# Kernel optimization log

Measured on AMD Instinct MI355X. Metric: run time of the kernel, lower is better.

Reference implementation:

```python
import jax, jax.numpy as jnp
import numpy as np

EPS = 1e-6
NUM_HEADS = 16

def _rmsnorm(h, w):
    hf = h.astype(jnp.float32)
    var = jnp.mean(hf * hf, axis=-1, keepdims=True)
    return (w * (hf * jax.lax.rsqrt(var + EPS))).astype(h.dtype)

def _rotary(t, cos, sin):
    # t: [B,N,H,hd]; cos/sin: [N, hd//2]
    tf = t.astype(jnp.float32)
    tr = tf[..., 0::2]
    ti = tf[..., 1::2]
    c = cos[None, :, None, :]
    s = sin[None, :, None, :]
    out_r = tr * c - ti * s
    out_i = tr * s + ti * c
    out = jnp.stack([out_r, out_i], axis=-1).reshape(t.shape)
    return out.astype(t.dtype)

def setup_inputs() -> dict:
    key = jax.random.key(0)
    ks = jax.random.split(key, 8)
    B, N, C = 2, 2048, 1024
    hd = C // NUM_HEADS
    x = jax.random.normal(ks[0], (B, N, C), jnp.float32)
    qkv_w = jax.random.normal(ks[1], (3 * C, C), jnp.float32) * (C ** -0.5)
    q_norm_w = jnp.ones((hd,), jnp.float32)
    k_norm_w = jnp.ones((hd,), jnp.float32)
    proj_w = jax.random.normal(ks[2], (C, C), jnp.float32) * (C ** -0.5)
    proj_b = jnp.zeros((C,), jnp.float32)
    # rotary freqs_cis = exp(i * theta): unit-magnitude cos/sin
    inv_freq = 1.0 / (10000.0 ** (jnp.arange(0, hd, 2, dtype=jnp.float32) / hd))
    ang = jnp.arange(N, dtype=jnp.float32)[:, None] * inv_freq[None, :]
    pos_cos = jnp.cos(ang)
    pos_sin = jnp.sin(ang)
    mask = jnp.tril(jnp.ones((N, N), dtype=bool))
    return {"x": x, "qkv_w": qkv_w, "q_norm_w": q_norm_w, "k_norm_w": k_norm_w,
            "proj_w": proj_w, "proj_b": proj_b, "pos_cos": pos_cos,
            "pos_sin": pos_sin, "mask": mask}

def reference(x, qkv_w, q_norm_w, k_norm_w, proj_w, proj_b, pos_cos, pos_sin, mask):
    B, N, C = x.shape
    H = NUM_HEADS
    hd = C // H
    qkv = (x @ qkv_w.T).reshape(B, N, 3, H, hd)
    q, k, v = qkv[:, :, 0], qkv[:, :, 1], qkv[:, :, 2]  # [B,N,H,hd]
    q = _rmsnorm(q, q_norm_w)
    k = _rmsnorm(k, k_norm_w)
    q = _rotary(q, pos_cos, pos_sin)
    k = _rotary(k, pos_cos, pos_sin)
    q = q.transpose(0, 2, 1, 3)  # [B,H,N,hd]
    k = k.transpose(0, 2, 1, 3)
    v = v.transpose(0, 2, 1, 3)
    scale = hd ** -0.5
    scores = jnp.einsum('bhqd,bhkd->bhqk', q, k) * scale
    scores = jnp.where(mask[None, None, :, :], scores, jnp.float32(-1e30))
    attn = jax.nn.softmax(scores, axis=-1)
    out = jnp.einsum('bhqk,bhkd->bhqd', attn, v)
    out = out.transpose(0, 2, 1, 3).reshape(B, N, C)
    return out @ proj_w.T + proj_b
```

## Files before the change

kernel.cpp:

```cpp
#include <hip/hip_runtime.h>

using u16 = unsigned short;
using short4v = __attribute__((ext_vector_type(4))) short;
using short8 = __attribute__((ext_vector_type(8))) short;
using floatx4 = __attribute__((ext_vector_type(4))) float;

__device__ __forceinline__ float bf2f(u16 h) {
  union { unsigned int u; float f; } v;
  v.u = ((unsigned int)h) << 16;
  return v.f;
}
__device__ __forceinline__ u16 f2bf(float f) {
  union { float f; unsigned int u; } v;
  v.f = f;
  unsigned int u = v.u;
  return (u16)((u + 0x7FFFu + ((u >> 16) & 1u)) >> 16);
}
__device__ __forceinline__ u16 f2bf_rtz(float f) {
  union { float f; unsigned int u; } v;
  v.f = f;
  return (u16)(v.u >> 16);
}

__device__ __forceinline__ float exp2_raw(float x) {
  return __builtin_amdgcn_exp2f(x);
}
__device__ __forceinline__ float rcp_raw(float x) {
  return __builtin_amdgcn_rcpf(x);
}

typedef const __attribute__((address_space(1))) unsigned int* gas_t;
typedef __attribute__((address_space(3))) unsigned int* las_t;
__device__ __forceinline__ void gl_lds16(const u16* g, u16* l) {
  __builtin_amdgcn_global_load_lds((gas_t)(const void*)g, (las_t)(void*)l, 16,
                                   0, 0);
}

#define MFMA32 __builtin_amdgcn_mfma_f32_16x16x32_bf16

#define QSCALE 0.180336880111f

__global__ __launch_bounds__(256) void cvt_all(
    const float* __restrict__ x, const float* __restrict__ wq,
    const float* __restrict__ wp, u16* __restrict__ xb, u16* __restrict__ wqb,
    u16* __restrict__ wpb) {
  int i = blockIdx.x * 256 + threadIdx.x;
  const float* src;
  u16* dst;
  int off;
  if (i < 1048576) {
    src = x; dst = xb; off = i;
  } else if (i < 1048576 + 786432) {
    src = wq; dst = wqb; off = i - 1048576;
  } else {
    src = wp; dst = wpb; off = i - 1835008;
  }
  float4 v = ((const float4*)src)[off];
  ushort4 o;
  o.x = f2bf(v.x);
  o.y = f2bf(v.y);
  o.z = f2bf(v.z);
  o.w = f2bf(v.w);
  ((ushort4*)dst)[off] = o;
}

template <int BIAS, int OUTBF16, int MT>
__global__ __launch_bounds__(256) void gemm_nt(
    const u16* __restrict__ A, const u16* __restrict__ B,
    const float* __restrict__ bias, void* __restrict__ Cout,
    int M, int N, int K) {
  constexpr int ROWS_A = MT * 32;
  __shared__ u16 As[ROWS_A * 64];
  __shared__ u16 Bs[128 * 64];
  const int tid = threadIdx.x;
  const int lane = tid & 63;
  const int wave = tid >> 6;
  const int col = lane & 15;
  const int quad = lane >> 4;
  const int bm = blockIdx.y * ROWS_A;
  const int bn = blockIdx.x * 128;
  const int wm = (wave >> 1) * (MT * 16);
  const int wn = (wave & 1) * 64;
  const int rsw = col & 7;

  floatx4 acc[MT][4] = {};

  for (int kb = 0; kb < K; kb += 64) {
    __syncthreads();
#pragma unroll
    for (int c = tid; c < ROWS_A * 8; c += 256) {
      const int row = c >> 3, s = (c & 7) ^ (row & 7);
      gl_lds16(A + (size_t)(bm + row) * K + kb + s * 8, As + c * 8);
    }
#pragma unroll
    for (int c = tid; c < 1024; c += 256) {
      const int row = c >> 3, s = (c & 7) ^ (row & 7);
      gl_lds16(B + (size_t)(bn + row) * K + kb + s * 8, Bs + c * 8);
    }
    __syncthreads();

#pragma unroll
    for (int kk = 0; kk < 2; kk++) {
      short8 af[MT], bfr[4];
#pragma unroll
      for (int i = 0; i < MT; i++)
        af[i] = *(const short8*)(As + (wm + i * 16 + col) * 64 +
                                 ((kk * 4 + quad) ^ rsw) * 8);
#pragma unroll
      for (int i = 0; i < 4; i++)
        bfr[i] = *(const short8*)(Bs + (wn + i * 16 + col) * 64 +
                                  ((kk * 4 + quad) ^ rsw) * 8);
#pragma unroll
      for (int mi = 0; mi < MT; mi++)
#pragma unroll
        for (int ni = 0; ni < 4; ni++)
          acc[mi][ni] = MFMA32(af[mi], bfr[ni], acc[mi][ni], 0, 0, 0);
    }
  }

#pragma unroll
  for (int mi = 0; mi < MT; mi++) {
#pragma unroll
    for (int ni = 0; ni < 4; ni++) {
#pragma unroll
      for (int r = 0; r < 4; r++) {
        int row = bm + wm + mi * 16 + quad * 4 + r;
        int c = bn + wn + ni * 16 + col;
        float v = acc[mi][ni][r];
        if (BIAS) v += bias[c];
        if (OUTBF16)
          ((u16*)Cout)[(size_t)row * N + c] = f2bf(v);
        else
          ((float*)Cout)[(size_t)row * N + c] = v;
      }
    }
  }
}

__global__ __launch_bounds__(256) void rope_v(
    const u16* __restrict__ qkv, const float* __restrict__ qw,
    const float* __restrict__ kw, const float* __restrict__ pcos,
    const float* __restrict__ psin, u16* __restrict__ Qb,
    u16* __restrict__ Kb, u16* __restrict__ Vt) {
  __shared__ u16 T[64 * 68];
  const int bh = blockIdx.x;
  const int n0 = blockIdx.y * 64;
  const int b = bh >> 4, h = bh & 15;
  const int tid = threadIdx.x;
  const int lane = tid & 63;
  const int wave = tid >> 6;

  const float qwl = qw[lane];
  const float kwl = kw[lane];
  for (int tt = 0; tt < 16; tt++) {
    const int n = n0 + wave * 16 + tt;
    const int t = b * 2048 + n;
    const u16* base = qkv + (size_t)t * 3072 + h * 64 + lane;
    float qv = bf2f(base[0]);
    float kv = bf2f(base[1024]);

    float sq = qv * qv, sk = kv * kv;
#pragma unroll
    for (int off = 32; off; off >>= 1) {
      sq += __shfl_xor(sq, off);
      sk += __shfl_xor(sk, off);
    }
    float qn = qv * rsqrtf(sq * (1.0f / 64.0f) + 1e-6f) * qwl;
    float kn = kv * rsqrtf(sk * (1.0f / 64.0f) + 1e-6f) * kwl;

    const int i = lane >> 1;
    const float c = pcos[n * 32 + i];
    const float s = psin[n * 32 + i];
    float qp = __shfl_xor(qn, 1);
    float kp = __shfl_xor(kn, 1);
    float qr, kr;
    if (lane & 1) {
      qr = qp * s + qn * c;
      kr = kp * s + kn * c;
    } else {
      qr = qn * c - qp * s;
      kr = kn * c - kp * s;
    }
    qr *= QSCALE;

    const size_t o = ((size_t)bh * 2048 + n) * 64 + lane;
    Qb[o] = f2bf(qr);
    Kb[o] = f2bf(kr);
  }

  const int q = tid & 7;
  const int r = tid >> 3;
#pragma unroll
  for (int rr = r; rr < 64; rr += 32) {
    short8 v = *(const short8*)(qkv + (size_t)(b * 2048 + n0 + rr) * 3072 +
                                2048 + h * 64 + q * 8);
    *(short8*)&T[rr * 68 + q * 8] = v;
  }
  __syncthreads();
#pragma unroll
  for (int dd = r; dd < 64; dd += 32) {
    short8 o;
#pragma unroll
    for (int j = 0; j < 8; j++) o[j] = T[(q * 8 + j) * 68 + dd];
    *(short8*)(Vt + (size_t)(bh * 64 + dd) * 2048 + n0 + q * 8) = o;
  }
}

__global__ __launch_bounds__(256) void attn_flash(
    const u16* __restrict__ Q, const u16* __restrict__ Kk,
    const u16* __restrict__ Vt, u16* __restrict__ O) {
  __shared__ u16 Ks[2][2][64 * 32];
  __shared__ u16 Vs[2][2][64 * 32];
  __shared__ u16 Pb[4][16 * 64];
  const int id = blockIdx.x;
  const int bh = id & 31;
  const int tile = 31 - (id >> 5);
  const int tid = threadIdx.x;
  const int lane = tid & 63;
  const int wave = tid >> 6;
  const int col = lane & 15;
  const int quad = lane >> 4;
  const int srow = tid >> 2;
  const int sswz = ((tid & 3) ^ (srow & 3)) * 8;
  const int rq = (quad ^ (col & 3)) * 8;
  const int pswz = (col & 7) << 1;

  const u16* Qh = Q + (size_t)bh * 2048 * 64;
  const u16* Kh = Kk + (size_t)bh * 2048 * 64;
  const u16* Vh = Vt + (size_t)bh * 64 * 2048;
  const int b = bh >> 4, h = bh & 15;

  const int q0 = tile * 64 + wave * 16;

  short8 aq[2];
#pragma unroll
  for (int ks = 0; ks < 2; ks++)
    aq[ks] = *(const short8*)(Qh + (size_t)(q0 + col) * 64 + ks * 32 + quad * 8);

  short8 ones;
#pragma unroll
  for (int j = 0; j < 8; j++) ones[j] = (short)0x3F80;

  floatx4 accO[4] = {};
  floatx4 lacc = {};
  const int nsteps = tile + 1;

#pragma unroll
  for (int half = 0; half < 2; half++) {
    gl_lds16(Kh + (size_t)srow * 64 + half * 32 + sswz,
             &Ks[0][half][0] + tid * 8);
    gl_lds16(Vh + (size_t)srow * 2048 + half * 32 + sswz,
             &Vs[0][half][0] + tid * 8);
  }
  __syncthreads();

  int cur = 0;
  for (int kt = 0; kt < nsteps; kt++) {
    const int j0 = kt * 64;

    if (kt + 1 < nsteps) {
      const int j1 = j0 + 64;
#pragma unroll
      for (int half = 0; half < 2; half++) {
        gl_lds16(Kh + (size_t)(j1 + srow) * 64 + half * 32 + sswz,
                 &Ks[cur ^ 1][half][0] + tid * 8);
        gl_lds16(Vh + (size_t)srow * 2048 + j1 + half * 32 + sswz,
                 &Vs[cur ^ 1][half][0] + tid * 8);
      }
    }

    floatx4 s[4] = {};
#pragma unroll
    for (int nt = 0; nt < 4; nt++) {
#pragma unroll
      for (int ks = 0; ks < 2; ks++) {
        short8 bk = *(const short8*)&Ks[cur][ks][(nt * 16 + col) * 32 + rq];
        s[nt] = MFMA32(bk, aq[ks], s[nt], 0, 0, 0);
      }
    }

    if (j0 + 63 <= q0) {
#pragma unroll
      for (int nt = 0; nt < 4; nt++) {
        short4v pk;
#pragma unroll
        for (int r = 0; r < 4; r++)
          pk[r] = (short)f2bf_rtz(exp2_raw(s[nt][r]));
        *(short4v*)&Pb[wave][col * 64 + ((nt * 4 + quad) ^ pswz) * 4] = pk;
      }
    } else {
      const int qg = q0 + col;
#pragma unroll
      for (int nt = 0; nt < 4; nt++) {
        const int jgb = j0 + nt * 16 + quad * 4;
        short4v pk;
#pragma unroll
        for (int r = 0; r < 4; r++) {
          float pv = (jgb + r <= qg) ? exp2_raw(s[nt][r]) : 0.0f;
          pk[r] = (short)f2bf_rtz(pv);
        }
        *(short4v*)&Pb[wave][col * 64 + ((nt * 4 + quad) ^ pswz) * 4] = pk;
      }
    }

    short8 ap[2];
#pragma unroll
    for (int kf = 0; kf < 2; kf++)
      ap[kf] = *(const short8*)&Pb[wave][col * 64 +
                                         ((kf * 8 + quad * 2) ^ pswz) * 4];

#pragma unroll
    for (int kf = 0; kf < 2; kf++)
      lacc = MFMA32(ap[kf], ones, lacc, 0, 0, 0);

#pragma unroll
    for (int nt = 0; nt < 4; nt++) {
#pragma unroll
      for (int kf = 0; kf < 2; kf++) {
        short8 bv = *(const short8*)&Vs[cur][kf][(nt * 16 + col) * 32 + rq];
        accO[nt] = MFMA32(ap[kf], bv, accO[nt], 0, 0, 0);
      }
    }

    __syncthreads();
    cur ^= 1;
  }

  float lrec[4];
#pragma unroll
  for (int r = 0; r < 4; r++) lrec[r] = rcp_raw(lacc[r]);

#pragma unroll
  for (int nt = 0; nt < 4; nt++) {
#pragma unroll
    for (int r = 0; r < 4; r++) {
      int qg = q0 + quad * 4 + r;
      int d = nt * 16 + col;
      O[((size_t)(b * 2048 + qg) * 16 + h) * 64 + d] =
          f2bf(accO[nt][r] * lrec[r]);
    }
  }
}

extern "C" void kernel_launch(void* const* d_in, const int* in_sizes, int n_in,
                              void* d_out, int out_size, void* d_ws,
                              size_t ws_size, hipStream_t stream) {
  const float* x = (const float*)d_in[0];
  const float* qkv_w = (const float*)d_in[1];
  const float* q_norm_w = (const float*)d_in[2];
  const float* k_norm_w = (const float*)d_in[3];
  const float* proj_w = (const float*)d_in[4];
  const float* proj_b = (const float*)d_in[5];
  const float* pos_cos = (const float*)d_in[6];
  const float* pos_sin = (const float*)d_in[7];

  char* ws = (char*)d_ws;
  u16* xb = (u16*)ws;
  u16* wqkvb = (u16*)(ws + 8388608);
  u16* wprojb = (u16*)(ws + 14680064);
  u16* qkv = (u16*)(ws + 16777216);
  u16* Qb = (u16*)(ws + 41943040);
  u16* Kb = (u16*)(ws + 50331648);
  u16* Vt = (u16*)(ws + 58720256);
  u16* AO = (u16*)(ws + 67108864);

  cvt_all<<<8192, 256, 0, stream>>>(x, qkv_w, proj_w, xb, wqkvb, wprojb);

  gemm_nt<0, 1, 4><<<dim3(24, 32), 256, 0, stream>>>(xb, wqkvb, nullptr, qkv,
                                                     4096, 3072, 1024);

  rope_v<<<dim3(32, 32), 256, 0, stream>>>(qkv, q_norm_w, k_norm_w, pos_cos,
                                           pos_sin, Qb, Kb, Vt);

  attn_flash<<<dim3(1024), 256, 0, stream>>>(Qb, Kb, Vt, AO);

  gemm_nt<1, 0, 2><<<dim3(8, 64), 256, 0, stream>>>(AO, wprojb, proj_b,
                                                    (float*)d_out, 4096, 1024,
                                                    1024);
}
```

Before: 199.4 us.

## Fuse RMSNorm, rotary and V transpose into QKV GEMM epilogue

Replaces the generic QKV GEMM plus separate rope_v kernel with a specialized GEMM whose epilogue does per-head RMSNorm via cross-lane shuffles, applies rotary embedding, scales Q, and writes Q/K in head-major layout and V transposed. This drops one kernel launch and the round trip of the intermediate qkv tensor through global memory. The cost is a heavier epilogue with scattered 2-byte stores and per-element cos/sin loads, which may be less coalesced than the old dedicated kernel.

```diff
diff --git a/kernel.cpp b/kernel.cpp
--- a/kernel.cpp
+++ b/kernel.cpp
@@ -137,72 +137,122 @@
   }
 }
 
-__global__ __launch_bounds__(256) void rope_v(
-    const u16* __restrict__ qkv, const float* __restrict__ qw,
-    const float* __restrict__ kw, const float* __restrict__ pcos,
-    const float* __restrict__ psin, u16* __restrict__ Qb,
-    u16* __restrict__ Kb, u16* __restrict__ Vt) {
-  __shared__ u16 T[64 * 68];
-  const int bh = blockIdx.x;
-  const int n0 = blockIdx.y * 64;
-  const int b = bh >> 4, h = bh & 15;
+__global__ __launch_bounds__(256) void gemm_qkv(
+    const u16* __restrict__ A, const u16* __restrict__ B,
+    const float* __restrict__ qw, const float* __restrict__ kw,
+    const float* __restrict__ pcos, const float* __restrict__ psin,
+    u16* __restrict__ Qb, u16* __restrict__ Kb, u16* __restrict__ Vt) {
+  constexpr int K = 1024;
+  __shared__ u16 As[128 * 64];
+  __shared__ u16 Bs[128 * 64];
   const int tid = threadIdx.x;
   const int lane = tid & 63;
   const int wave = tid >> 6;
-
-  const float qwl = qw[lane];
-  const float kwl = kw[lane];
-  for (int tt = 0; tt < 16; tt++) {
-    const int n = n0 + wave * 16 + tt;
-    const int t = b * 2048 + n;
-    const u16* base = qkv + (size_t)t * 3072 + h * 64 + lane;
-    float qv = bf2f(base[0]);
-    float kv = bf2f(base[1024]);
-
-    float sq = qv * qv, sk = kv * kv;
-#pragma unroll
-    for (int off = 32; off; off >>= 1) {
-      sq += __shfl_xor(sq, off);
-      sk += __shfl_xor(sk, off);
-    }
-    float qn = qv * rsqrtf(sq * (1.0f / 64.0f) + 1e-6f) * qwl;
-    float kn = kv * rsqrtf(sk * (1.0f / 64.0f) + 1e-6f) * kwl;
-
-    const int i = lane >> 1;
-    const float c = pcos[n * 32 + i];
-    const float s = psin[n * 32 + i];
-    float qp = __shfl_xor(qn, 1);
-    float kp = __shfl_xor(kn, 1);
-    float qr, kr;
-    if (lane & 1) {
-      qr = qp * s + qn * c;
-      kr = kp * s + kn * c;
-    } else {
-      qr = qn * c - qp * s;
-      kr = kn * c - kp * s;
-    }
-    qr *= QSCALE;
-
-    const size_t o = ((size_t)bh * 2048 + n) * 64 + lane;
-    Qb[o] = f2bf(qr);
-    Kb[o] = f2bf(kr);
-  }
-
-  const int q = tid & 7;
-  const int r = tid >> 3;
-#pragma unroll
-  for (int rr = r; rr < 64; rr += 32) {
-    short8 v = *(const short8*)(qkv + (size_t)(b * 2048 + n0 + rr) * 3072 +
-                                2048 + h * 64 + q * 8);
-    *(short8*)&T[rr * 68 + q * 8] = v;
-  }
-  __syncthreads();
-#pragma unroll
-  for (int dd = r; dd < 64; dd += 32) {
-    short8 o;
-#pragma unroll
-    for (int j = 0; j < 8; j++) o[j] = T[(q * 8 + j) * 68 + dd];
-    *(short8*)(Vt + (size_t)(bh * 64 + dd) * 2048 + n0 + q * 8) = o;
+  const int col = lane & 15;
+  const int quad = lane >> 4;
+  const int bm = blockIdx.y * 128;
+  const int bn = blockIdx.x * 128;
+  const int wm = (wave >> 1) * 64;
+  const int wn = (wave & 1) * 64;
+  const int rsw = col & 7;
+
+  floatx4 acc[4][4] = {};
+
+  for (int kb = 0; kb < K; kb += 64) {
+    __syncthreads();
+#pragma unroll
+    for (int c = tid; c < 1024; c += 256) {
+      const int row = c >> 3, s = (c & 7) ^ (row & 7);
+      gl_lds16(A + (size_t)(bm + row) * K + kb + s * 8, As + c * 8);
+    }
+#pragma unroll
+    for (int c = tid; c < 1024; c += 256) {
+      const int row = c >> 3, s = (c & 7) ^ (row & 7);
+      gl_lds16(B + (size_t)(bn + row) * K + kb + s * 8, Bs + c * 8);
+    }
+    __syncthreads();
+
+#pragma unroll
+    for (int kk = 0; kk < 2; kk++) {
+      short8 af[4], bfr[4];
+#pragma unroll
+      for (int i = 0; i < 4; i++)
+        af[i] = *(const short8*)(As + (wm + i * 16 + col) * 64 +
+                                 ((kk * 4 + quad) ^ rsw) * 8);
+#pragma unroll
+      for (int i = 0; i < 4; i++)
+        bfr[i] = *(const short8*)(Bs + (wn + i * 16 + col) * 64 +
+                                  ((kk * 4 + quad) ^ rsw) * 8);
+#pragma unroll
+      for (int mi = 0; mi < 4; mi++)
+#pragma unroll
+        for (int ni = 0; ni < 4; ni++)
+          acc[mi][ni] = MFMA32(af[mi], bfr[ni], acc[mi][ni], 0, 0, 0);
+    }
+  }
+
+  const int c0 = bn + wn;
+  const int type = c0 >> 10;
+  const int h = (c0 >> 6) & 15;
+  const int b = bm >> 11;
+  const int bh = b * 16 + h;
+  const int nt0 = (bm & 2047) + wm;
+
+  if (type == 2) {
+#pragma unroll
+    for (int mi = 0; mi < 4; mi++) {
+#pragma unroll
+      for (int ni = 0; ni < 4; ni++) {
+        const int d = ni * 16 + col;
+        const int n0 = nt0 + mi * 16 + quad * 4;
+        short4v pk;
+#pragma unroll
+        for (int r = 0; r < 4; r++) pk[r] = (short)f2bf(acc[mi][ni][r]);
+        *(short4v*)&Vt[((size_t)(bh * 64 + d)) * 2048 + n0] = pk;
+      }
+    }
+  } else {
+    u16* const dst = type ? Kb : Qb;
+    const float* const nw = type ? kw : qw;
+    float wloc[4];
+#pragma unroll
+    for (int ni = 0; ni < 4; ni++) wloc[ni] = nw[ni * 16 + col];
+
+#pragma unroll
+    for (int mi = 0; mi < 4; mi++) {
+      floatx4 ss = {};
+#pragma unroll
+      for (int ni = 0; ni < 4; ni++)
+#pragma unroll
+        for (int r = 0; r < 4; r++) ss[r] += acc[mi][ni][r] * acc[mi][ni][r];
+#pragma unroll
+      for (int off = 1; off <= 8; off <<= 1)
+#pragma unroll
+        for (int r = 0; r < 4; r++) ss[r] += __shfl_xor(ss[r], off);
+      floatx4 rn;
+#pragma unroll
+      for (int r = 0; r < 4; r++)
+        rn[r] = rsqrtf(ss[r] * (1.0f / 64.0f) + 1e-6f);
+
+#pragma unroll
+      for (int ni = 0; ni < 4; ni++) {
+        float nv[4], pv[4];
+#pragma unroll
+        for (int r = 0; r < 4; r++) nv[r] = acc[mi][ni][r] * rn[r] * wloc[ni];
+#pragma unroll
+        for (int r = 0; r < 4; r++) pv[r] = __shfl_xor(nv[r], 1);
+#pragma unroll
+        for (int r = 0; r < 4; r++) {
+          const int n = nt0 + mi * 16 + quad * 4 + r;
+          const float cc = pcos[n * 32 + ni * 8 + (col >> 1)];
+          const float sn = psin[n * 32 + ni * 8 + (col >> 1)];
+          float out = (col & 1) ? pv[r] * sn + nv[r] * cc
+                                : nv[r] * cc - pv[r] * sn;
+          if (type == 0) out *= QSCALE;
+          dst[((size_t)(bh * 2048 + n)) * 64 + ni * 16 + col] = f2bf(out);
+        }
+      }
+    }
   }
 }
 
@@ -358,7 +408,6 @@
   u16* xb = (u16*)ws;
   u16* wqkvb = (u16*)(ws + 8388608);
   u16* wprojb = (u16*)(ws + 14680064);
-  u16* qkv = (u16*)(ws + 16777216);
   u16* Qb = (u16*)(ws + 41943040);
   u16* Kb = (u16*)(ws + 50331648);
   u16* Vt = (u16*)(ws + 58720256);
@@ -366,11 +415,8 @@
 
   cvt_all<<<8192, 256, 0, stream>>>(x, qkv_w, proj_w, xb, wqkvb, wprojb);
 
-  gemm_nt<0, 1, 4><<<dim3(24, 32), 256, 0, stream>>>(xb, wqkvb, nullptr, qkv,
-                                                     4096, 3072, 1024);
-
-  rope_v<<<dim3(32, 32), 256, 0, stream>>>(qkv, q_norm_w, k_norm_w, pos_cos,
-                                           pos_sin, Qb, Kb, Vt);
+  gemm_qkv<<<dim3(24, 32), 256, 0, stream>>>(xb, wqkvb, q_norm_w, k_norm_w,
+                                             pos_cos, pos_sin, Qb, Kb, Vt);
 
   attn_flash<<<dim3(1024), 256, 0, stream>>>(Qb, Kb, Vt, AO);
 
```

After: 199.4 us. Within noise of the previous version (+0.0%).
